# Performance work log

Hardware: AMD Instinct MI355X
Metric: run time of the kernel (lower is better)

Reference implementation:

```python
import jax, jax.numpy as jnp
import numpy as np

NX, DX, H, DO = 8192, 8, 1024, 1


def setup_inputs() -> dict:
    key = jax.random.key(0)
    ks = jax.random.split(key, 7)
    s1 = 1.0 / np.sqrt(DX)  # torch Linear default init bound
    s2 = 1.0 / np.sqrt(H)
    x = jax.random.normal(ks[0], (NX, DX), jnp.float32)
    W1 = jax.random.uniform(ks[1], (H, DX), jnp.float32, -s1, s1)
    b1 = jax.random.uniform(ks[2], (H,), jnp.float32, -s1, s1)
    W2 = jax.random.uniform(ks[3], (H, H), jnp.float32, -s2, s2)
    b2 = jax.random.uniform(ks[4], (H,), jnp.float32, -s2, s2)
    W3 = jax.random.uniform(ks[5], (DO, H), jnp.float32, -s2, s2)
    b3 = jax.random.uniform(ks[6], (DO,), jnp.float32, -s2, s2)
    return {"x": x, "W1": W1, "b1": b1, "W2": W2, "b2": b2, "W3": W3, "b3": b3}


def reference(x, W1, b1, W2, b2, W3, b3):
    # Forward: Linear -> Tanh -> Linear -> Tanh -> Linear
    z1 = jnp.tanh(x @ W1.T + b1)          # [nx, h]
    z2 = jnp.tanh(z1 @ W2.T + b2)         # [nx, h]
    y = z2 @ W3.T + b3                    # [nx, out]

    # DerivTanh(h) = 4/(e^-h + e^h)^2 = sech^2(h) = 1 - tanh(h)^2
    d1 = 1.0 - z1 * z1                    # [nx, h]
    d2 = 1.0 - z2 * z2                    # [nx, h]

    # Vectorized analytic Jacobian (original loops over each input dim k):
    # tmp_k = d2 * (W2 @ (d1 * W1[:, k]))  then  dydx_k = W3 @ tmp_k
    J = d1[:, :, None] * W1[None, :, :]                    # [nx, h, dx]
    J = d2[:, :, None] * jnp.einsum('ij,njk->nik', W2, J)  # [nx, h, dx]
    dydx = jnp.einsum('oj,njk->nok', W3, J)                # [nx, out, dx]
    # Match original list-of-dx ordering: dydx[k] has shape [nx, out]
    dydx = jnp.transpose(dydx, (2, 0, 1))                  # [dx, nx, out]
    return y, dydx
```

## Files before the change

kernel.cpp:

```cpp
#include <hip/hip_runtime.h>
#include <stdint.h>

#define NXS 8192
#define HS  1024

typedef __attribute__((ext_vector_type(8))) short short8;
typedef __attribute__((ext_vector_type(4))) float f32x4;

__device__ __forceinline__ float bf2f(uint32_t b) {
    union { uint32_t u; float f; } c; c.u = b << 16; return c.f;
}
__device__ __forceinline__ uint16_t f2bf(float f) {
    union { float f; uint32_t u; } c; c.f = f;
    return (uint16_t)((c.u + 0x7fffu + ((c.u >> 16) & 1u)) >> 16);
}
__device__ __forceinline__ float fast_tanh(float x) {
    float xc = fminf(fmaxf(x, -15.f), 15.f);
    return 1.f - __fdividef(2.f, __expf(2.f * xc) + 1.f);
}
__device__ __forceinline__ void async_cp16(const void* g, void* l) {
    __builtin_amdgcn_global_load_lds(
        (const __attribute__((address_space(1))) void*)g,
        (__attribute__((address_space(3))) void*)l,
        16, 0, 0);
}

__global__ __launch_bounds__(256) void k01(
    const float* __restrict__ x, const float* __restrict__ W1,
    const float* __restrict__ b1, const float* __restrict__ W2,
    const float* __restrict__ b3, uint16_t* __restrict__ Z1,
    uint16_t* __restrict__ Bp1, uint16_t* __restrict__ Bp2,
    uint16_t* __restrict__ W1T, float* __restrict__ out)
{
    __shared__ float xs[8][8];
    const int b = blockIdx.x, t = threadIdx.x;
    if (b < 1024) {
        const int n0 = b * 8;
        if (t < 64) xs[t >> 3][t & 7] = x[n0 * 8 + t];
        const int j = t * 4;
        float w[4][8];
#pragma unroll
        for (int c = 0; c < 4; ++c) {
            float4 w0 = *(const float4*)(W1 + (j + c) * 8);
            float4 w1 = *(const float4*)(W1 + (j + c) * 8 + 4);
            w[c][0] = w0.x; w[c][1] = w0.y; w[c][2] = w0.z; w[c][3] = w0.w;
            w[c][4] = w1.x; w[c][5] = w1.y; w[c][6] = w1.z; w[c][7] = w1.w;
        }
        float4 bb = *(const float4*)(b1 + j);
        const float bv[4] = {bb.x, bb.y, bb.z, bb.w};
        __syncthreads();
#pragma unroll
        for (int s = 0; s < 8; ++s) {
            ushort4 o;
            uint16_t* op = (uint16_t*)&o;
#pragma unroll
            for (int c = 0; c < 4; ++c) {
                float sum = bv[c];
#pragma unroll
                for (int k = 0; k < 8; ++k) sum += xs[s][k] * w[c][k];
                op[c] = f2bf(fast_tanh(sum));
            }
            *(ushort4*)(Z1 + (size_t)(n0 + s) * HS + j) = o;
        }
    } else if (b < 1536) {
        const int tid = (b - 1024) * 256 + t;
        const int l = tid & 63, c = (tid >> 6) & 31, g = tid >> 11;
        const int lr = l & 15, lq = l >> 4;
        const float* src = W2 + (size_t)(g * 16 + lr) * HS + c * 32 + lq * 8;
        float4 a0 = *(const float4*)src;
        float4 a1 = *(const float4*)(src + 4);
        uint16_t o[8];
        o[0] = f2bf(a0.x); o[1] = f2bf(a0.y); o[2] = f2bf(a0.z); o[3] = f2bf(a0.w);
        o[4] = f2bf(a1.x); o[5] = f2bf(a1.y); o[6] = f2bf(a1.z); o[7] = f2bf(a1.w);
        *(ushort4*)(Bp1 + (size_t)tid * 8)     = *(ushort4*)&o[0];
        *(ushort4*)(Bp1 + (size_t)tid * 8 + 4) = *(ushort4*)&o[4];
    } else if (b < 2048) {
        const int tid = (b - 1536) * 256 + t;
        const int l = tid & 63, c = (tid >> 6) & 31, g = tid >> 11;
        const int lr = l & 15, lq = l >> 4;
        uint16_t o[8];
#pragma unroll
        for (int j2 = 0; j2 < 8; ++j2)
            o[j2] = f2bf(W2[(size_t)(c * 32 + lq * 8 + j2) * HS + g * 16 + lr]);
        *(ushort4*)(Bp2 + (size_t)tid * 8)     = *(ushort4*)&o[0];
        *(ushort4*)(Bp2 + (size_t)tid * 8 + 4) = *(ushort4*)&o[4];
    } else if (b < 2336) {
        const int idx = (b - 2048) * 256 + t;
        out[idx] = (idx < NXS) ? b3[0] : 0.f;
    } else {
        const int idx = (b - 2336) * 256 + t;
        const int r = idx >> 10, cc = idx & 1023;
        W1T[idx] = (r < 8) ? f2bf(W1[cc * 8 + r]) : (uint16_t)0;
    }
}

template <int MODE>
__global__ __launch_bounds__(256, 2) void gemm_k(
    const uint16_t* __restrict__ A, const uint16_t* __restrict__ Bp,
    const float* __restrict__ bias, const float* __restrict__ W3,
    uint16_t* __restrict__ Out, float* __restrict__ yOut,
    const uint16_t* __restrict__ Z1, const uint16_t* __restrict__ W1T,
    float* __restrict__ dOut)
{
    __shared__ __attribute__((aligned(16))) uint16_t smem[24576];
    const int t = threadIdx.x;
    const int wave = t >> 6, lane = t & 63;
    const int lq = lane >> 4, lr = lane & 15;
    const int wr = wave >> 1, wc = wave & 1;
    const int rowBase = blockIdx.x * 128;
    const int colBase = blockIdx.y * 128;

    const uint16_t* gA0;
    const uint16_t* gA1;
    {
        int s0 = t,       r0 = s0 >> 2, q0 = (s0 & 3) ^ ((r0 >> 1) & 3);
        int s1 = t + 256, r1 = s1 >> 2, q1 = (s1 & 3) ^ ((r1 >> 1) & 3);
        gA0 = A + (size_t)(rowBase + r0) * HS + q0 * 8;
        gA1 = A + (size_t)(rowBase + r1) * HS + q1 * 8;
    }
    const uint16_t* gB0;
    const uint16_t* gB1;
    {
        int s0 = t, s1 = t + 256;
        gB0 = Bp + ((size_t)(colBase >> 4) + (s0 >> 6)) * 16384 + (size_t)(s0 & 63) * 8;
        gB1 = Bp + ((size_t)(colBase >> 4) + (s1 >> 6)) * 16384 + (size_t)(s1 & 63) * 8;
    }
    const int ldsA0 = t * 16;
    const int ldsA1 = t * 16 + 4096;
    const int ldsB0 = t * 16 + 8192;
    const int ldsB1 = t * 16 + 12288;

    float cB[4], cW[4]; int cCol[4];
    if (MODE == 0) {
#pragma unroll
        for (int tj = 0; tj < 4; ++tj) {
            cCol[tj] = colBase + wc * 64 + tj * 16 + lr;
            cB[tj] = bias[cCol[tj]];
            cW[tj] = W3[cCol[tj]];
        }
    }

    f32x4 acc[4][4] = {};

    async_cp16(gA0,        (char*)smem + ldsA0);
    async_cp16(gA1,        (char*)smem + ldsA1);
    async_cp16(gB0,        (char*)smem + ldsB0);
    async_cp16(gB1,        (char*)smem + ldsB1);
    async_cp16(gA0 + 32,   (char*)smem + 16384 + ldsA0);
    async_cp16(gA1 + 32,   (char*)smem + 16384 + ldsA1);
    async_cp16(gB0 + 512,  (char*)smem + 16384 + ldsB0);
    async_cp16(gB1 + 512,  (char*)smem + 16384 + ldsB1);
    gA0 += 64; gA1 += 64; gB0 += 1024; gB1 += 1024;
    asm volatile("s_waitcnt vmcnt(4)" ::: "memory");
    __builtin_amdgcn_s_barrier();

    int rb = 0, wb = 2;
#pragma unroll 1
    for (int c = 0; c < 32; ++c) {
        if (c < 30) {
            char* d = (char*)smem + wb * 16384;
            async_cp16(gA0, d + ldsA0);
            async_cp16(gA1, d + ldsA1);
            async_cp16(gB0, d + ldsB0);
            async_cp16(gB1, d + ldsB1);
            gA0 += 32; gA1 += 32; gB0 += 512; gB1 += 512;
            asm volatile("" ::: "memory");
        }
        const uint16_t* pA  = smem + rb * 8192;
        const uint16_t* pBl = pA + 4096;
        short8 bfrag[4];
#pragma unroll
        for (int tj = 0; tj < 4; ++tj)
            bfrag[tj] = *(const short8*)(pBl + (((wc << 2) + tj) * 64 + lane) * 8);
        short8 af[4];
#pragma unroll
        for (int ti = 0; ti < 4; ++ti) {
            int ar = wr * 64 + ti * 16 + lr;
            af[ti] = *(const short8*)(pA + ar * 32
                      + ((lq ^ ((ar >> 1) & 3)) << 3));
        }
        __builtin_amdgcn_s_setprio(1);
#pragma unroll
        for (int ti = 0; ti < 4; ++ti)
#pragma unroll
            for (int tj = 0; tj < 4; ++tj)
                acc[ti][tj] = __builtin_amdgcn_mfma_f32_16x16x32_bf16(
                    af[ti], bfrag[tj], acc[ti][tj], 0, 0, 0);
        __builtin_amdgcn_s_setprio(0);
        if (c < 30) {
            asm volatile("s_waitcnt vmcnt(4)" ::: "memory");
        } else {
            asm volatile("s_waitcnt vmcnt(0)" ::: "memory");
        }
        __builtin_amdgcn_s_barrier();
        rb = (rb == 2) ? 0 : rb + 1;
        wb = (wb == 2) ? 0 : wb + 1;
    }

    if (MODE == 0) {
#pragma unroll
        for (int ti = 0; ti < 4; ++ti) {
#pragma unroll
            for (int r = 0; r < 4; ++r) {
                int row = rowBase + wr * 64 + ti * 16 + lq * 4 + r;
                float ys = 0.f;
#pragma unroll
                for (int tj = 0; tj < 4; ++tj) {
                    float z2 = fast_tanh(acc[ti][tj][r] + cB[tj]);
                    ys += z2 * cW[tj];
                    Out[(size_t)row * HS + cCol[tj]] = f2bf((1.f - z2 * z2) * cW[tj]);
                }
                ys += __shfl_xor(ys, 1); ys += __shfl_xor(ys, 2);
                ys += __shfl_xor(ys, 4); ys += __shfl_xor(ys, 8);
                if (lr == 0) atomicAdd(&yOut[row], ys);
            }
        }
    } else {
        __builtin_amdgcn_sched_barrier(0);
#pragma unroll
        for (int ti = 0; ti < 4; ++ti)
#pragma unroll
            for (int r = 0; r < 4; ++r) {
                int rowl = wr * 64 + ti * 16 + lq * 4 + r;
                const size_t zrow = (size_t)(rowBase + rowl) * HS + colBase;
#pragma unroll
                for (int tj = 0; tj < 4; ++tj) {
                    int coll = wc * 64 + tj * 16 + lr;
                    float z1 = bf2f(Z1[zrow + coll]);
                    smem[rowl * 136 + coll] =
                        f2bf(acc[ti][tj][r] * (1.f - z1 * z1));
                }
            }
        __syncthreads();
        f32x4 dd[2] = {};
#pragma unroll
        for (int h = 0; h < 2; ++h)
#pragma unroll
            for (int kb = 0; kb < 4; ++kb) {
                short8 aF = *(const short8*)(smem + (wave * 32 + h * 16 + lr) * 136
                                             + kb * 32 + lq * 8);
                short8 bF = *(const short8*)(W1T + (size_t)lr * HS + colBase
                                             + kb * 32 + lq * 8);
                dd[h] = __builtin_amdgcn_mfma_f32_16x16x32_bf16(aF, bF, dd[h], 0, 0, 0);
            }
        if (lr < 8) {
#pragma unroll
            for (int h = 0; h < 2; ++h) {
                int row = rowBase + wave * 32 + h * 16 + lq * 4;
#pragma unroll
                for (int rg = 0; rg < 4; ++rg)
                    atomicAdd(&dOut[(size_t)lr * NXS + row + rg], dd[h][rg]);
            }
        }
    }
}

extern "C" void kernel_launch(void* const* d_in, const int* in_sizes, int n_in,
                              void* d_out, int out_size, void* d_ws, size_t ws_size,
                              hipStream_t stream) {
    (void)in_sizes; (void)n_in; (void)out_size; (void)ws_size;
    const float* x  = (const float*)d_in[0];
    const float* W1 = (const float*)d_in[1];
    const float* b1 = (const float*)d_in[2];
    const float* W2 = (const float*)d_in[3];
    const float* b2 = (const float*)d_in[4];
    const float* W3 = (const float*)d_in[5];
    const float* b3 = (const float*)d_in[6];
    float* out = (float*)d_out;

    char* ws = (char*)d_ws;
    uint16_t* Z1  = (uint16_t*)(ws);
    uint16_t* V   = (uint16_t*)(ws + (size_t)16 * 1024 * 1024);
    uint16_t* Bp1 = (uint16_t*)(ws + (size_t)32 * 1024 * 1024);
    uint16_t* Bp2 = (uint16_t*)(ws + (size_t)34 * 1024 * 1024);
    uint16_t* W1T = (uint16_t*)(ws + (size_t)36 * 1024 * 1024);

    k01<<<2400, 256, 0, stream>>>(x, W1, b1, W2, b3, Z1, Bp1, Bp2, W1T, out);
    gemm_k<0><<<dim3(NXS / 128, HS / 128), 256, 0, stream>>>(
        Z1, Bp1, b2, W3, V, out, nullptr, nullptr, nullptr);
    gemm_k<1><<<dim3(NXS / 128, HS / 128), 256, 0, stream>>>(
        V, Bp2, nullptr, nullptr, nullptr, nullptr, Z1, W1T, out + NXS);
}
```

Measured before the change: 133.2 us.

## Load GEMM B fragments straight into registers and double-buffer them across unrolled steps

The B operand no longer goes through LDS. Each wave now reads its pre-packed B fragments directly from global memory into registers, double-buffered (bX/bY) across a main loop unrolled by two. LDS then holds only A tiles in four 8 KB slots, which shrinks the shared allocation and removes the LDS write/read round-trip for B. In exchange, waves that share columns each fetch the same B data, adding L2 traffic. The loop also drops its explicit vmcnt waits and relies on ordering from the compiler-inserted waits for the B register loads, which is a correctness risk for the async A copies.

New measurement: 138.6 us. +4.0%, slower.

```diff
diff --git a/kernel.cpp b/kernel.cpp
--- a/kernel.cpp
+++ b/kernel.cpp
@@ -23,6 +23,11 @@
         (const __attribute__((address_space(1))) void*)g,
         (__attribute__((address_space(3))) void*)l,
         16, 0, 0);
+}
+__device__ __forceinline__ void mem_barrier() {
+    asm volatile("" ::: "memory");
+    __builtin_amdgcn_s_barrier();
+    asm volatile("" ::: "memory");
 }
 
 __global__ __launch_bounds__(256) void k01(
@@ -102,7 +107,7 @@
     const uint16_t* __restrict__ Z1, const uint16_t* __restrict__ W1T,
     float* __restrict__ dOut)
 {
-    __shared__ __attribute__((aligned(16))) uint16_t smem[24576];
+    __shared__ __attribute__((aligned(16))) uint16_t smem[17408];
     const int t = threadIdx.x;
     const int wave = t >> 6, lane = t & 63;
     const int lq = lane >> 4, lr = lane & 15;
@@ -118,17 +123,14 @@
         gA0 = A + (size_t)(rowBase + r0) * HS + q0 * 8;
         gA1 = A + (size_t)(rowBase + r1) * HS + q1 * 8;
     }
-    const uint16_t* gB0;
-    const uint16_t* gB1;
-    {
-        int s0 = t, s1 = t + 256;
-        gB0 = Bp + ((size_t)(colBase >> 4) + (s0 >> 6)) * 16384 + (size_t)(s0 & 63) * 8;
-        gB1 = Bp + ((size_t)(colBase >> 4) + (s1 >> 6)) * 16384 + (size_t)(s1 & 63) * 8;
-    }
     const int ldsA0 = t * 16;
     const int ldsA1 = t * 16 + 4096;
-    const int ldsB0 = t * 16 + 8192;
-    const int ldsB1 = t * 16 + 12288;
+
+    const uint16_t* pB[4];
+#pragma unroll
+    for (int tj = 0; tj < 4; ++tj)
+        pB[tj] = Bp + ((size_t)(colBase >> 4) + wc * 4 + tj) * 16384
+                    + (size_t)lane * 8;
 
     float cB[4], cW[4]; int cCol[4];
     if (MODE == 0) {
@@ -141,61 +143,73 @@
     }
 
     f32x4 acc[4][4] = {};
-
-    async_cp16(gA0,        (char*)smem + ldsA0);
-    async_cp16(gA1,        (char*)smem + ldsA1);
-    async_cp16(gB0,        (char*)smem + ldsB0);
-    async_cp16(gB1,        (char*)smem + ldsB1);
-    async_cp16(gA0 + 32,   (char*)smem + 16384 + ldsA0);
-    async_cp16(gA1 + 32,   (char*)smem + 16384 + ldsA1);
-    async_cp16(gB0 + 512,  (char*)smem + 16384 + ldsB0);
-    async_cp16(gB1 + 512,  (char*)smem + 16384 + ldsB1);
-    gA0 += 64; gA1 += 64; gB0 += 1024; gB1 += 1024;
+    short8 bX[4], bY[4];
+
+    async_cp16(gA0,      (char*)smem + ldsA0);
+    async_cp16(gA1,      (char*)smem + ldsA1);
+    async_cp16(gA0 + 32, (char*)smem + 8192 + ldsA0);
+    async_cp16(gA1 + 32, (char*)smem + 8192 + ldsA1);
+    asm volatile("" ::: "memory");
+#pragma unroll
+    for (int tj = 0; tj < 4; ++tj)
+        bX[tj] = *(const short8*)(pB[tj]);
     asm volatile("s_waitcnt vmcnt(4)" ::: "memory");
     __builtin_amdgcn_s_barrier();
-
-    int rb = 0, wb = 2;
+    asm volatile("" ::: "memory");
+
+#define COMPUTE(bufByte, breg)                                               \
+    {                                                                        \
+        const uint16_t* pA_ = (const uint16_t*)((const char*)smem + (bufByte)); \
+        short8 af_[4];                                                       \
+        _Pragma("unroll")                                                    \
+        for (int ti_ = 0; ti_ < 4; ++ti_) {                                  \
+            int ar_ = wr * 64 + ti_ * 16 + lr;                               \
+            af_[ti_] = *(const short8*)(pA_ + ar_ * 32                       \
+                        + ((lq ^ ((ar_ >> 1) & 3)) << 3));                   \
+        }                                                                    \
+        _Pragma("unroll")                                                    \
+        for (int ti_ = 0; ti_ < 4; ++ti_)                                    \
+            _Pragma("unroll")                                                \
+            for (int tj_ = 0; tj_ < 4; ++tj_)                                \
+                acc[ti_][tj_] = __builtin_amdgcn_mfma_f32_16x16x32_bf16(     \
+                    af_[ti_], breg[tj_], acc[ti_][tj_], 0, 0, 0);            \
+    }
+
 #pragma unroll 1
-    for (int c = 0; c < 32; ++c) {
-        if (c < 30) {
-            char* d = (char*)smem + wb * 16384;
-            async_cp16(gA0, d + ldsA0);
-            async_cp16(gA1, d + ldsA1);
-            async_cp16(gB0, d + ldsB0);
-            async_cp16(gB1, d + ldsB1);
-            gA0 += 32; gA1 += 32; gB0 += 512; gB1 += 512;
+    for (int i = 0; i < 16; ++i) {
+        const int c = 2 * i;
+        const int bEven = (i & 1) * 16384;
+        const int bOdd  = bEven + 8192;
+        const int bNx2  = ((i & 1) ^ 1) * 16384;
+        const int bNx3  = bNx2 + 8192;
+
+        if (c + 2 < 32) {
+            async_cp16(gA0 + (c + 2) * 32, (char*)smem + bNx2 + ldsA0);
+            async_cp16(gA1 + (c + 2) * 32, (char*)smem + bNx2 + ldsA1);
             asm volatile("" ::: "memory");
         }
-        const uint16_t* pA  = smem + rb * 8192;
-        const uint16_t* pBl = pA + 4096;
-        short8 bfrag[4];
-#pragma unroll
-        for (int tj = 0; tj < 4; ++tj)
-            bfrag[tj] = *(const short8*)(pBl + (((wc << 2) + tj) * 64 + lane) * 8);
-        short8 af[4];
-#pragma unroll
-        for (int ti = 0; ti < 4; ++ti) {
-            int ar = wr * 64 + ti * 16 + lr;
-            af[ti] = *(const short8*)(pA + ar * 32
-                      + ((lq ^ ((ar >> 1) & 3)) << 3));
-        }
-        __builtin_amdgcn_s_setprio(1);
-#pragma unroll
-        for (int ti = 0; ti < 4; ++ti)
+        if (c + 1 < 32) {
 #pragma unroll
             for (int tj = 0; tj < 4; ++tj)
-                acc[ti][tj] = __builtin_amdgcn_mfma_f32_16x16x32_bf16(
-                    af[ti], bfrag[tj], acc[ti][tj], 0, 0, 0);
-        __builtin_amdgcn_s_setprio(0);
-        if (c < 30) {
-            asm volatile("s_waitcnt vmcnt(4)" ::: "memory");
-        } else {
-            asm volatile("s_waitcnt vmcnt(0)" ::: "memory");
-        }
-        __builtin_amdgcn_s_barrier();
-        rb = (rb == 2) ? 0 : rb + 1;
-        wb = (wb == 2) ? 0 : wb + 1;
-    }
+                bY[tj] = *(const short8*)(pB[tj] + (c + 1) * 512);
+        }
+        COMPUTE(bEven, bX)
+        mem_barrier();
+
+        if (c + 3 < 32) {
+            async_cp16(gA0 + (c + 3) * 32, (char*)smem + bNx3 + ldsA0);
+            async_cp16(gA1 + (c + 3) * 32, (char*)smem + bNx3 + ldsA1);
+            asm volatile("" ::: "memory");
+        }
+        if (c + 2 < 32) {
+#pragma unroll
+            for (int tj = 0; tj < 4; ++tj)
+                bX[tj] = *(const short8*)(pB[tj] + (c + 2) * 512);
+        }
+        COMPUTE(bOdd, bY)
+        mem_barrier();
+    }
+#undef COMPUTE
 
     if (MODE == 0) {
 #pragma unroll
@@ -216,7 +230,6 @@
             }
         }
     } else {
-        __builtin_amdgcn_sched_barrier(0);
 #pragma unroll
         for (int ti = 0; ti < 4; ++ti)
 #pragma unroll
```
